# Kernel optimization log

Measured on AMD Instinct MI355X. Metric: run time of the kernel, lower is better.

## Reference

```python
import jax, jax.numpy as jnp
import numpy as np

N = 50000      # nodes
D = 256        # hid_size (span_emb_size)
DH = D // 2    # per-direction GNN output
V = 2          # num_views = len(retypes)
E = 800000     # edges per view per direction (avg degree 16)


def _gnn(x, edges, W, b):
    """Mean-aggregation GCN message passing: h_dst = relu(mean_{src->dst} x_src @ W + b)."""
    src, dst = edges[0], edges[1]
    msg = x[src] @ W                                   # [E, DH] gather + GEMM
    agg = jax.ops.segment_sum(msg, dst, num_segments=N)
    deg = jax.ops.segment_sum(jnp.ones((msg.shape[0],), x.dtype), dst, num_segments=N)
    return jax.nn.relu(agg / jnp.maximum(deg, 1.0)[:, None] + b)


def setup_inputs() -> dict:
    key = jax.random.key(0)
    ks = jax.random.split(key, 10)
    inps = jax.random.normal(ks[0], (N, D), dtype=jnp.float32)
    fw_edges = jax.random.randint(ks[1], (V, 2, E), 0, N, dtype=jnp.int32)
    bw_edges = jax.random.randint(ks[2], (V, 2, E), 0, N, dtype=jnp.int32)
    s = 1.0 / np.sqrt(D)
    W_fw = jax.random.uniform(ks[3], (V, D, DH), jnp.float32, -s, s)
    b_fw = jax.random.uniform(ks[4], (V, DH), jnp.float32, -s, s)
    W_bw = jax.random.uniform(ks[5], (V, D, DH), jnp.float32, -s, s)
    b_bw = jax.random.uniform(ks[6], (V, DH), jnp.float32, -s, s)
    W1 = jax.random.uniform(ks[7], (D, D), jnp.float32, -s, s)
    b1 = jax.random.uniform(ks[8], (D,), jnp.float32, -s, s)
    return {"inps": inps, "fw_edges": fw_edges, "bw_edges": bw_edges,
            "W_fw": W_fw, "b_fw": b_fw, "W_bw": W_bw, "b_bw": b_bw,
            "W1": W1, "b1": b1}


def reference(inps, fw_edges, bw_edges, W_fw, b_fw, W_bw, b_bw, W1, b1):
    # dropout is identity at inference (p applied only in training)
    acc = jnp.zeros_like(inps)
    for v in range(V):  # small fixed number of structurally distinct views
        fw_o = _gnn(inps, fw_edges[v], W_fw[v], b_fw[v])   # [N, DH]
        bw_o = _gnn(inps, bw_edges[v], W_bw[v], b_bw[v])   # [N, DH]
        acc = acc + jnp.concatenate([bw_o, fw_o], axis=-1)  # [N, D], summed over views
    feats = jax.nn.relu(acc) @ W1 + b1 + inps               # act -> linear1 -> residual
    return feats
```

## Files before the change

### kernel.cpp

```cpp
#include <hip/hip_runtime.h>

#define D_ 256
#define DH_ 128
#define NBMAX 128
#define BCAP 9216

using bf16x8 = __attribute__((ext_vector_type(8))) short;
using f32x4  = __attribute__((ext_vector_type(4))) float;
using f32x2  = __attribute__((ext_vector_type(2))) float;

__device__ __forceinline__ unsigned short f2bf(float f) {
  unsigned int u = __builtin_bit_cast(unsigned int, f);
  u += 0x7fffu + ((u >> 16) & 1u);
  return (unsigned short)(u >> 16);
}
__device__ __forceinline__ unsigned char f2fp8(float f) {
  unsigned int pk = __builtin_amdgcn_cvt_pk_fp8_f32(f, 0.f, 0u, false);
  return (unsigned char)(pk & 0xffu);
}


__global__ __launch_bounds__(512) void part_k(const int* __restrict__ fw,
                                              const int* __restrict__ bw,
                                              int* __restrict__ gcnt,
                                              unsigned int* __restrict__ buckets,
                                              int E_, int nb) {
  __shared__ int hist[NBMAX];
  __shared__ int gbase[NBMAX];
  int g = blockIdx.y;
  const int* src = (g < 2 ? fw : bw) + (size_t)(g & 1) * 2 * E_;
  const int* dst = src + E_;
  int t = threadIdx.x;
  for (int i = t; i < nb; i += 512) hist[i] = 0;
  __syncthreads();
  int base = blockIdx.x * 8192;
  unsigned int pk[16];
  int lp[16];
#pragma unroll
  for (int j = 0; j < 16; ++j) {
    int e = base + j * 512 + t;
    if (e < E_) {
      int s = src[e], d = dst[e];
      pk[j] = (unsigned int)s | ((unsigned int)d << 16);
      lp[j] = atomicAdd(&hist[d >> 9], 1);
    } else {
      pk[j] = 0u; lp[j] = -1;
    }
  }
  __syncthreads();
  for (int i = t; i < nb; i += 512) gbase[i] = atomicAdd(&gcnt[g * NBMAX + i], hist[i]);
  __syncthreads();
#pragma unroll
  for (int j = 0; j < 16; ++j) {
    if (lp[j] >= 0) {
      int b = pk[j] >> 25;
      int pos = gbase[b] + lp[j];
      if (pos < BCAP) buckets[((size_t)(g * NBMAX + b)) * BCAP + pos] = pk[j];
    }
  }
}

__global__ __launch_bounds__(256) void csr_k(const unsigned int* __restrict__ buckets,
                                             const int* __restrict__ gcnt,
                                             int* __restrict__ deg, int* __restrict__ offs,
                                             int* __restrict__ csr, int N_, int E_) {
  __shared__ int ldeg[512];
  __shared__ int loff[512];
  __shared__ int wsum[4];
  __shared__ int red[4];
  int g = blockIdx.y, b = blockIdx.x;
  int t = threadIdx.x;
  int lane = t & 63, w = t >> 6;
  int cnt = min(gcnt[g * NBMAX + b], BCAP);
  const unsigned int* ebuf = buckets + ((size_t)(g * NBMAX + b)) * BCAP;
  int nodebase = b << 9;
  int nloc = min(512, N_ - nodebase);
  for (int i = t; i < 512; i += 256) ldeg[i] = 0;
  int val = (t < b) ? min(gcnt[g * NBMAX + t], BCAP) : 0;
  for (int o = 1; o < 64; o <<= 1) val += __shfl_xor(val, o, 64);
  if (lane == 0) red[w] = val;
  __syncthreads();
  int gb = red[0] + red[1] + red[2] + red[3];
  for (int i = t; i < cnt; i += 256) atomicAdd(&ldeg[(ebuf[i] >> 16) & 511], 1);
  __syncthreads();
  int i0 = w * 128 + lane * 2;
  int a0 = ldeg[i0], a1 = ldeg[i0 + 1];
  int pair = a0 + a1, incl = pair;
  for (int o = 1; o < 64; o <<= 1) {
    int x = __shfl_up(incl, o, 64);
    if (lane >= o) incl += x;
  }
  if (lane == 63) wsum[w] = incl;
  __syncthreads();
  int wpre = 0;
  for (int k = 0; k < w; ++k) wpre += wsum[k];
  int e0 = wpre + incl - pair;
  loff[i0] = e0;
  loff[i0 + 1] = e0 + a0;
  __syncthreads();
  for (int i = t; i < nloc; i += 256) {
    deg[(size_t)g * N_ + nodebase + i] = ldeg[i];
    offs[(size_t)g * N_ + nodebase + i] = gb + loff[i];
  }
  for (int i = t; i < 512; i += 256) ldeg[i] = 0;
  __syncthreads();
  int* csrg = csr + (size_t)g * E_ + gb;
  for (int i = t; i < cnt; i += 256) {
    unsigned int pk = ebuf[i];
    int d = (pk >> 16) & 511;
    int lp = atomicAdd(&ldeg[d], 1);
    csrg[loff[d] + lp] = (int)(pk & 0xffffu);
  }
}


__global__ void prepw_k(const float* __restrict__ Wfw, const float* __restrict__ Wbw,
                        const float* __restrict__ W1,
                        unsigned short* __restrict__ Wt, unsigned short* __restrict__ W1t,
                        int* __restrict__ gcnt) {
  int i = blockIdx.x * blockDim.x + threadIdx.x;
  if (i < 4 * NBMAX) gcnt[i] = 0;
  const int nw = 4 * D_ * DH_;
  if (i < nw) {
    int g = i >> 15;
    int r = i & 32767;
    int n = r >> 8, k = r & 255;
    const float* W = (g < 2 ? Wfw : Wbw) + (size_t)(g & 1) * D_ * DH_;
    Wt[i] = f2bf(W[k * DH_ + n]);
  } else if (i < nw + D_ * D_) {
    int r = i - nw;
    int c = r >> 8, k = r & 255;
    W1t[r] = f2bf(W1[k * D_ + c]);
  }
}


__global__ __launch_bounds__(256) void ygemm_k(const float* __restrict__ x,
                                               const unsigned short* __restrict__ Wt,
                                               unsigned char* __restrict__ y, int N_) {
  __shared__ unsigned short At[32 * 256];
  int t = threadIdx.x, lane = t & 63, w = t >> 6;
  int tile = blockIdx.x;
#pragma unroll
  for (int it = 0; it < 8; ++it) {
    int idx = it * 256 + t;
    int row = idx >> 6, slot = idx & 63;
    int gr = tile * 32 + row;
    float4 v = {0.f, 0.f, 0.f, 0.f};
    if (gr < N_) v = ((const float4*)x)[(size_t)gr * 64 + slot];
    int c = slot * 4;
    int sc2 = (c & 7) | ((((c >> 3)) ^ (row & 7)) << 3);
    ushort4 o;
    o.x = f2bf(v.x); o.y = f2bf(v.y); o.z = f2bf(v.z); o.w = f2bf(v.w);
    *(ushort4*)&At[row * 256 + sc2] = o;
  }
  __syncthreads();
  int krow = (lane >> 4) * 8;
  for (int g = 0; g < 4; ++g) {
    f32x4 acc[2][2];
#pragma unroll
    for (int a = 0; a < 2; ++a)
#pragma unroll
      for (int b = 0; b < 2; ++b) acc[a][b] = (f32x4){0.f, 0.f, 0.f, 0.f};
    const unsigned short* Wg = Wt + (size_t)g * (DH_ * D_);
#pragma unroll
    for (int kk = 0; kk < 8; ++kk) {
      bf16x8 afr[2];
#pragma unroll
      for (int rt = 0; rt < 2; ++rt) {
        int r = rt * 16 + (lane & 15);
        int cc = kk * 32 + krow;
        afr[rt] = *(const bf16x8*)&At[r * 256 + (cc ^ ((r & 7) << 3))];
      }
#pragma unroll
      for (int ct2 = 0; ct2 < 2; ++ct2) {
        int n = w * 32 + ct2 * 16 + (lane & 15);
        bf16x8 bfr = *(const bf16x8*)(Wg + (size_t)n * 256 + kk * 32 + krow);
#pragma unroll
        for (int rt = 0; rt < 2; ++rt)
          acc[rt][ct2] = __builtin_amdgcn_mfma_f32_16x16x32_bf16(afr[rt], bfr, acc[rt][ct2], 0, 0, 0);
      }
    }
#pragma unroll
    for (int ct2 = 0; ct2 < 2; ++ct2)
#pragma unroll
      for (int rt = 0; rt < 2; ++rt)
#pragma unroll
        for (int j = 0; j < 4; ++j) {
          int row = tile * 32 + rt * 16 + (lane >> 4) * 4 + j;
          int col = w * 32 + ct2 * 16 + (lane & 15);
          if (row < N_) y[((size_t)g * N_ + row) * DH_ + col] = f2fp8(acc[rt][ct2][j]);
        }
  }
}


__device__ __forceinline__ void acc2(f32x2* s, uint2 q) {
  s[0] += __builtin_amdgcn_cvt_pk_f32_fp8(q.x, false);
  s[1] += __builtin_amdgcn_cvt_pk_f32_fp8(q.x, true);
  s[2] += __builtin_amdgcn_cvt_pk_f32_fp8(q.y, false);
  s[3] += __builtin_amdgcn_cvt_pk_f32_fp8(q.y, true);
}

#define GATHER(sacc, dgv, offv, gidx)                                                   \
  {                                                                                     \
    const int* lst = csr + (size_t)(gidx) * E_ + (offv);                                \
    const unsigned char* yg = y + (size_t)(gidx) * N_ * DH_;                            \
    int jend = (dgv) & ~3;                                                              \
    int j = 0;                                                                          \
    _Pragma("unroll 1")                                                                 \
    for (; j < jend; j += 4) {                                                          \
      int4 iv = *(const int4*)(lst + j);                                                \
      uint2 q0 = *(const uint2*)(yg + ((((unsigned)iv.x & 0xffffu) << 7) + boff));      \
      uint2 q1 = *(const uint2*)(yg + ((((unsigned)iv.y & 0xffffu) << 7) + boff));      \
      uint2 q2 = *(const uint2*)(yg + ((((unsigned)iv.z & 0xffffu) << 7) + boff));      \
      uint2 q3 = *(const uint2*)(yg + ((((unsigned)iv.w & 0xffffu) << 7) + boff));      \
      acc2(sacc, q0); acc2(sacc, q1); acc2(sacc, q2); acc2(sacc, q3);                   \
    }                                                                                   \
    if (j < (dgv)) {                                                                    \
      int4 iv = *(const int4*)(lst + j);                                                \
      uint2 q0 = *(const uint2*)(yg + ((((unsigned)iv.x & 0xffffu) << 7) + boff));      \
      uint2 q1 = *(const uint2*)(yg + ((((unsigned)iv.y & 0xffffu) << 7) + boff));      \
      uint2 q2 = *(const uint2*)(yg + ((((unsigned)iv.z & 0xffffu) << 7) + boff));      \
      if (j + 0 < (dgv)) acc2(sacc, q0);                                                \
      if (j + 1 < (dgv)) acc2(sacc, q1);                                                \
      if (j + 2 < (dgv)) acc2(sacc, q2);                                                \
    }                                                                                   \
  }

__global__ __launch_bounds__(256, 6) void gnn2_k(
    const unsigned char* __restrict__ y,
    const int* __restrict__ deg, const int* __restrict__ offs, const int* __restrict__ csr,
    const float* __restrict__ bias_fw, const float* __restrict__ bias_bw,
    unsigned short* __restrict__ accb, int N_, int E_) {
  const int tid = threadIdx.x;
  const int lane = tid & 63, w = tid >> 6;
  const int grp = lane >> 4, l15 = lane & 15;
  const int tile = blockIdx.x, dir = blockIdx.y;
  const int colbase = dir ? 0 : 128;
  const float* bias = dir ? bias_bw : bias_fw;
  const unsigned boff = l15 * 8;
  const int g0 = dir * 2, g1 = g0 + 1;

#pragma unroll 1
  for (int rr = 0; rr < 2; ++rr) {
    int nd = tile * 32 + rr * 16 + w * 4 + grp;
    bool act = nd < N_;
    int nds = act ? nd : 0;
    f32x2 s0[4], s1[4];
#pragma unroll
    for (int k = 0; k < 4; ++k) { s0[k] = (f32x2){0.f, 0.f}; s1[k] = (f32x2){0.f, 0.f}; }
    int dg0 = deg[(size_t)g0 * N_ + nds];
    int off0 = offs[(size_t)g0 * N_ + nds];
    int dg1 = deg[(size_t)g1 * N_ + nds];
    int off1 = offs[(size_t)g1 * N_ + nds];
    if (!act) { dg0 = 0; dg1 = 0; }

    GATHER(s0, dg0, off0, g0);
    GATHER(s1, dg1, off1, g1);

    float sc0 = 1.0f / (float)max(dg0, 1);
    float sc1 = 1.0f / (float)max(dg1, 1);
    const float* bp0 = bias + boff;
    const float* bp1 = bias + DH_ + boff;
    uint4 pk;
    unsigned* pw = (unsigned*)&pk;
#pragma unroll
    for (int k = 0; k < 4; ++k) {
      float h0 = fmaxf(s0[k].x * sc0 + bp0[2 * k],     0.f) + fmaxf(s1[k].x * sc1 + bp1[2 * k],     0.f);
      float h1 = fmaxf(s0[k].y * sc0 + bp0[2 * k + 1], 0.f) + fmaxf(s1[k].y * sc1 + bp1[2 * k + 1], 0.f);
      pw[k] = (unsigned)f2bf(h0) | ((unsigned)f2bf(h1) << 16);
    }
    if (act) *(uint4*)(accb + (size_t)nd * 256 + colbase + boff) = pk;
  }
}


__global__ __launch_bounds__(256) void gemm2_k(
    const unsigned short* __restrict__ accb, const unsigned short* __restrict__ W1t,
    const float* __restrict__ b1, const float* __restrict__ x,
    float* __restrict__ out, int N_) {
  int tid = threadIdx.x;
  int lane = tid & 63, w = tid >> 6;
  int tile = blockIdx.x;
  f32x4 acc[2][4];
#pragma unroll
  for (int a = 0; a < 2; ++a)
#pragma unroll
    for (int b = 0; b < 4; ++b) acc[a][b] = (f32x4){0.f, 0.f, 0.f, 0.f};
  int krow = (lane >> 4) * 8;
#pragma unroll
  for (int kk = 0; kk < 8; ++kk) {
    bf16x8 afr[2];
#pragma unroll
    for (int rt = 0; rt < 2; ++rt) {
      int row = tile * 32 + rt * 16 + (lane & 15);
      row = min(row, N_ - 1);
      afr[rt] = *(const bf16x8*)(accb + (size_t)row * 256 + kk * 32 + krow);
    }
#pragma unroll
    for (int ct = 0; ct < 4; ++ct) {
      int cn = w * 64 + ct * 16 + (lane & 15);
      bf16x8 bfr = *(const bf16x8*)(W1t + (size_t)cn * 256 + kk * 32 + krow);
#pragma unroll
      for (int rt = 0; rt < 2; ++rt)
        acc[rt][ct] = __builtin_amdgcn_mfma_f32_16x16x32_bf16(afr[rt], bfr, acc[rt][ct], 0, 0, 0);
    }
  }
#pragma unroll
  for (int ct = 0; ct < 4; ++ct) {
    int col = w * 64 + ct * 16 + (lane & 15);
    float bb = b1[col];
#pragma unroll
    for (int rt = 0; rt < 2; ++rt)
#pragma unroll
      for (int j = 0; j < 4; ++j) {
        int row = tile * 32 + rt * 16 + (lane >> 4) * 4 + j;
        if (row < N_)
          out[(size_t)row * 256 + col] = acc[rt][ct][j] + bb + x[(size_t)row * 256 + col];
      }
  }
}


extern "C" void kernel_launch(void* const* d_in, const int* in_sizes, int n_in,
                              void* d_out, int out_size, void* d_ws, size_t ws_size,
                              hipStream_t stream) {
  const float* inps = (const float*)d_in[0];
  const int* fw = (const int*)d_in[1];
  const int* bw = (const int*)d_in[2];
  const float* Wfw = (const float*)d_in[3];
  const float* bfw = (const float*)d_in[4];
  const float* Wbw = (const float*)d_in[5];
  const float* bbw = (const float*)d_in[6];
  const float* W1 = (const float*)d_in[7];
  const float* b1 = (const float*)d_in[8];
  float* out = (float*)d_out;

  int N_ = in_sizes[0] / D_;
  int E_ = in_sizes[1] / 4;
  int nb = (N_ + 511) >> 9;

  char* ws = (char*)d_ws;
  size_t p = 0;
  int* deg = (int*)(ws + p);              p += (size_t)4 * N_ * 4;
  int* offs = (int*)(ws + p);             p += (size_t)4 * N_ * 4;
  int* gcnt = (int*)(ws + p);             p += (size_t)4 * NBMAX * 4;
  int* csr = (int*)(ws + p);              p += (size_t)4 * E_ * 4;
  unsigned int* buckets = (unsigned int*)(ws + p);  p += (size_t)4 * NBMAX * BCAP * 4;
  unsigned short* Wt = (unsigned short*)(ws + p);   p += (size_t)4 * D_ * DH_ * 2;
  unsigned short* W1t = (unsigned short*)(ws + p);  p += (size_t)D_ * D_ * 2;
  unsigned char* y = (unsigned char*)(ws + p);      p += (size_t)4 * N_ * DH_;
  unsigned short* accb = (unsigned short*)(ws + p); p += (size_t)N_ * D_ * 2;

  prepw_k<<<768, 256, 0, stream>>>(Wfw, Wbw, W1, Wt, W1t, gcnt);

  int ntiles = (N_ + 31) / 32;
  ygemm_k<<<ntiles, 256, 0, stream>>>(inps, Wt, y, N_);

  dim3 pgrid((E_ + 8191) / 8192, 4);
  part_k<<<pgrid, 512, 0, stream>>>(fw, bw, gcnt, buckets, E_, nb);
  dim3 cgrid(nb, 4);
  csr_k<<<cgrid, 256, 0, stream>>>(buckets, gcnt, deg, offs, csr, N_, E_);

  dim3 ggrid(ntiles, 2);
  gnn2_k<<<ggrid, 256, 0, stream>>>(y, deg, offs, csr, bfw, bbw, accb, N_, E_);
  gemm2_k<<<ntiles, 256, 0, stream>>>(accb, W1t, b1, inps, out, N_);
}
```

Before: 240.5 us.

## Restructure ygemm to compute all four weight groups per k-step and stage gemm2 A-tile in LDS

In ygemm_k the outer loop over the four weight groups is folded into the k loop. Each k-step loads the A fragment from shared memory once and issues all 16 MFMAs against batched B fragments, with accumulators for all groups held in registers. gemm2_k now stages its 32x256 bf16 activation tile in swizzled LDS with coalesced loads instead of strided per-lane global reads. B loads are batched before the MFMAs and launch bounds gain occupancy hints, trading higher register pressure and possible spills for better memory-level parallelism.

```diff
diff --git a/kernel.cpp b/kernel.cpp
--- a/kernel.cpp
+++ b/kernel.cpp
@@ -135,9 +135,9 @@
 }
 
 
-__global__ __launch_bounds__(256) void ygemm_k(const float* __restrict__ x,
-                                               const unsigned short* __restrict__ Wt,
-                                               unsigned char* __restrict__ y, int N_) {
+__global__ __launch_bounds__(256, 3) void ygemm_k(const float* __restrict__ x,
+                                                  const unsigned short* __restrict__ Wt,
+                                                  unsigned char* __restrict__ y, int N_) {
   __shared__ unsigned short At[32 * 256];
   int t = threadIdx.x, lane = t & 63, w = t >> 6;
   int tile = blockIdx.x;
@@ -156,31 +156,41 @@
   }
   __syncthreads();
   int krow = (lane >> 4) * 8;
-  for (int g = 0; g < 4; ++g) {
-    f32x4 acc[2][2];
+  int l15 = lane & 15;
+  f32x4 acc[4][2][2];
+#pragma unroll
+  for (int g = 0; g < 4; ++g)
 #pragma unroll
     for (int a = 0; a < 2; ++a)
 #pragma unroll
-      for (int b = 0; b < 2; ++b) acc[a][b] = (f32x4){0.f, 0.f, 0.f, 0.f};
-    const unsigned short* Wg = Wt + (size_t)g * (DH_ * D_);
-#pragma unroll
-    for (int kk = 0; kk < 8; ++kk) {
-      bf16x8 afr[2];
-#pragma unroll
-      for (int rt = 0; rt < 2; ++rt) {
-        int r = rt * 16 + (lane & 15);
-        int cc = kk * 32 + krow;
-        afr[rt] = *(const bf16x8*)&At[r * 256 + (cc ^ ((r & 7) << 3))];
+      for (int b = 0; b < 2; ++b) acc[g][a][b] = (f32x4){0.f, 0.f, 0.f, 0.f};
+#pragma unroll
+  for (int kk = 0; kk < 8; ++kk) {
+    bf16x8 afr[2];
+#pragma unroll
+    for (int rt = 0; rt < 2; ++rt) {
+      int r = rt * 16 + l15;
+      int cc = kk * 32 + krow;
+      afr[rt] = *(const bf16x8*)&At[r * 256 + (cc ^ ((r & 7) << 3))];
+    }
+    bf16x8 bfr[4][2];
+#pragma unroll
+    for (int g = 0; g < 4; ++g)
+#pragma unroll
+      for (int ct2 = 0; ct2 < 2; ++ct2) {
+        int n = w * 32 + ct2 * 16 + l15;
+        bfr[g][ct2] = *(const bf16x8*)(Wt + (size_t)g * (DH_ * D_) + (size_t)n * 256 + kk * 32 + krow);
       }
 #pragma unroll
-      for (int ct2 = 0; ct2 < 2; ++ct2) {
-        int n = w * 32 + ct2 * 16 + (lane & 15);
-        bf16x8 bfr = *(const bf16x8*)(Wg + (size_t)n * 256 + kk * 32 + krow);
+    for (int g = 0; g < 4; ++g)
+#pragma unroll
+      for (int ct2 = 0; ct2 < 2; ++ct2)
 #pragma unroll
         for (int rt = 0; rt < 2; ++rt)
-          acc[rt][ct2] = __builtin_amdgcn_mfma_f32_16x16x32_bf16(afr[rt], bfr, acc[rt][ct2], 0, 0, 0);
-      }
-    }
+          acc[g][rt][ct2] = __builtin_amdgcn_mfma_f32_16x16x32_bf16(afr[rt], bfr[g][ct2], acc[g][rt][ct2], 0, 0, 0);
+  }
+#pragma unroll
+  for (int g = 0; g < 4; ++g)
 #pragma unroll
     for (int ct2 = 0; ct2 < 2; ++ct2)
 #pragma unroll
@@ -188,10 +198,9 @@
 #pragma unroll
         for (int j = 0; j < 4; ++j) {
           int row = tile * 32 + rt * 16 + (lane >> 4) * 4 + j;
-          int col = w * 32 + ct2 * 16 + (lane & 15);
-          if (row < N_) y[((size_t)g * N_ + row) * DH_ + col] = f2fp8(acc[rt][ct2][j]);
+          int col = w * 32 + ct2 * 16 + l15;
+          if (row < N_) y[((size_t)g * N_ + row) * DH_ + col] = f2fp8(acc[g][rt][ct2][j]);
         }
-  }
 }
 
 
@@ -276,13 +285,25 @@
 }
 
 
-__global__ __launch_bounds__(256) void gemm2_k(
+__global__ __launch_bounds__(256, 4) void gemm2_k(
     const unsigned short* __restrict__ accb, const unsigned short* __restrict__ W1t,
     const float* __restrict__ b1, const float* __restrict__ x,
     float* __restrict__ out, int N_) {
+  __shared__ unsigned short Bt[32 * 256];
   int tid = threadIdx.x;
   int lane = tid & 63, w = tid >> 6;
+  int l15 = lane & 15;
   int tile = blockIdx.x;
+#pragma unroll
+  for (int it = 0; it < 4; ++it) {
+    int idx = it * 256 + tid;
+    int row = idx >> 5, slot = idx & 31;
+    int gr = min(tile * 32 + row, N_ - 1);
+    uint4 v = *(const uint4*)(accb + (size_t)gr * 256 + slot * 8);
+    int c = slot * 8;
+    *(uint4*)&Bt[row * 256 + (c ^ ((row & 7) << 3))] = v;
+  }
+  __syncthreads();
   f32x4 acc[2][4];
 #pragma unroll
   for (int a = 0; a < 2; ++a)
@@ -294,22 +315,25 @@
     bf16x8 afr[2];
 #pragma unroll
     for (int rt = 0; rt < 2; ++rt) {
-      int row = tile * 32 + rt * 16 + (lane & 15);
-      row = min(row, N_ - 1);
-      afr[rt] = *(const bf16x8*)(accb + (size_t)row * 256 + kk * 32 + krow);
-    }
+      int r = rt * 16 + l15;
+      int cc = kk * 32 + krow;
+      afr[rt] = *(const bf16x8*)&Bt[r * 256 + (cc ^ ((r & 7) << 3))];
+    }
+    bf16x8 bfr[4];
 #pragma unroll
     for (int ct = 0; ct < 4; ++ct) {
-      int cn = w * 64 + ct * 16 + (lane & 15);
-      bf16x8 bfr = *(const bf16x8*)(W1t + (size_t)cn * 256 + kk * 32 + krow);
+      int cn = w * 64 + ct * 16 + l15;
+      bfr[ct] = *(const bf16x8*)(W1t + (size_t)cn * 256 + kk * 32 + krow);
+    }
+#pragma unroll
+    for (int ct = 0; ct < 4; ++ct)
 #pragma unroll
       for (int rt = 0; rt < 2; ++rt)
-        acc[rt][ct] = __builtin_amdgcn_mfma_f32_16x16x32_bf16(afr[rt], bfr, acc[rt][ct], 0, 0, 0);
-    }
+        acc[rt][ct] = __builtin_amdgcn_mfma_f32_16x16x32_bf16(afr[rt], bfr[ct], acc[rt][ct], 0, 0, 0);
   }
 #pragma unroll
   for (int ct = 0; ct < 4; ++ct) {
-    int col = w * 64 + ct * 16 + (lane & 15);
+    int col = w * 64 + ct * 16 + l15;
     float bb = b1[col];
 #pragma unroll
     for (int rt = 0; rt < 2; ++rt)
```

Measured after the change: 238.1 us. No clear change (-1.0%).
